# Kernel optimization log

Measured on AMD Instinct MI355X. Metric: run time of the kernel, lower is better.

## Reference

```python
import jax, jax.numpy as jnp
import numpy as np

B, C, H, W = 64, 256, 56, 56
SCALES = (1, 2, 4, 8)  # scale[:groups] with groups=4; sum = 15 pooled maps


def setup_inputs() -> dict:
    key = jax.random.key(0)
    k1, k2 = jax.random.split(key)
    x = jax.random.normal(k1, (B, C, H, W), dtype=jnp.float32)
    # weight: [num_fea=H*W, sum(scales)=15]; small init (original fills 0, which
    # would make the gate identically sigmoid(0)=0.5 — use small random instead)
    weight = jax.random.normal(k2, (H * W, 15), dtype=jnp.float32) * 0.02
    return {"x": x, "weight": weight}


def reference(x, weight):
    b, c, h, w = x.shape
    hw = h * w
    # Multi-scale channel-group mean pooling: for scale i, split channels into
    # i equal groups (c divisible by all scales) and mean over each group.
    # Equivalent to the original's loop of c*j//i : c*(j+1)//i slices.
    feats = [x.reshape(b, i, c // i, hw).mean(axis=2) for i in SCALES]
    t = jnp.concatenate(feats, axis=1)  # [b, 15, hw]
    # Points(): normalize across the 15 pooled features per spatial location
    mean = t.mean(axis=1, keepdims=True)           # [b, 1, hw]
    std = t.std(axis=1, keepdims=True)             # unbiased=False (ddof=0)
    tn = (t - mean) / std                          # [b, 15, hw]
    # _style_integration: per-pixel weighted sum over the 15 features
    z = jnp.einsum('bfs,sf->bs', tn, weight)       # [b, hw]
    gate = jax.nn.sigmoid(z).reshape(b, 1, h, w)
    return x * gate
```

## Files before the change

kernel.cpp:

```cpp
#include <hip/hip_runtime.h>
#include <math.h>


constexpr int C_   = 256;
constexpr int HW_  = 3136;
constexpr int T_   = 64;
constexpr int TPB_ = HW_ / T_;
constexpr int B_   = 64;

__global__ __launch_bounds__(256, 2) void ppca_fused(
    const float* __restrict__ x, const float* __restrict__ wgt,
    float* __restrict__ out)
{
  __shared__ __align__(16) float tile[C_ * T_];
  __shared__ float S[8 * T_];
  __shared__ float gate[T_];

  const int blk = blockIdx.x;
  const int b   = blk / TPB_;
  const int til = blk - b * TPB_;
  const int sp0 = til * T_;
  const size_t base = (size_t)b * C_ * HW_ + sp0;
  const float* xb = x + base;
  float* ob = out + base;

  const int t   = threadIdx.x;
  const int sp4 = t & 15;
  const int c0  = t >> 4;

  float4 v[16];
  #pragma unroll
  for (int i = 0; i < 16; ++i) {
    const int c = c0 + (i << 4);
    v[i] = *(const float4*)(xb + (size_t)c * HW_ + (sp4 << 2));
  }
  #pragma unroll
  for (int i = 0; i < 16; ++i) {
    const int c = c0 + (i << 4);
    *(float4*)(&tile[c * T_ + (sp4 << 2)]) = v[i];
  }
  __syncthreads();

  {
    const int w = t >> 6;
    const int l = t & 63;
    float s0 = 0.f, s1 = 0.f;
    #pragma unroll
    for (int k = 0; k < 32; ++k) s0 += tile[(w * 64 + k) * T_ + l];
    #pragma unroll
    for (int k = 0; k < 32; ++k) s1 += tile[(w * 64 + 32 + k) * T_ + l];
    S[(2 * w) * T_ + l]     = s0;
    S[(2 * w + 1) * T_ + l] = s1;
  }
  __syncthreads();

  if (t < T_) {
    float Sg[8];
    #pragma unroll
    for (int g = 0; g < 8; ++g) Sg[g] = S[g * T_ + t];
    float p64[4];
    #pragma unroll
    for (int j = 0; j < 4; ++j) p64[j] = Sg[2 * j] + Sg[2 * j + 1];
    const float p128a = p64[0] + p64[1];
    const float p128b = p64[2] + p64[3];
    const float tot   = p128a + p128b;

    float f[15];
    f[0] = tot * (1.f / 256.f);
    f[1] = p128a * (1.f / 128.f);
    f[2] = p128b * (1.f / 128.f);
    #pragma unroll
    for (int j = 0; j < 4; ++j) f[3 + j] = p64[j] * (1.f / 64.f);
    #pragma unroll
    for (int g = 0; g < 8; ++g) f[7 + g] = Sg[g] * (1.f / 32.f);

    float m = 0.f;
    #pragma unroll
    for (int i = 0; i < 15; ++i) m += f[i];
    m *= (1.f / 15.f);
    float var = 0.f;
    #pragma unroll
    for (int i = 0; i < 15; ++i) { const float d = f[i] - m; var += d * d; }
    var *= (1.f / 15.f);
    const float inv = 1.f / sqrtf(var);

    const float* wp = wgt + (size_t)(sp0 + t) * 15;
    float z = 0.f;
    #pragma unroll
    for (int i = 0; i < 15; ++i) z += (f[i] - m) * wp[i];
    z *= inv;
    gate[t] = 1.f / (1.f + __expf(-z));
  }
  __syncthreads();

  const float4 g4 = *(const float4*)(&gate[sp4 << 2]);
  #pragma unroll
  for (int i = 0; i < 16; ++i) {
    const int c = c0 + (i << 4);
    float4 vv = *(const float4*)(&tile[c * T_ + (sp4 << 2)]);
    vv.x *= g4.x; vv.y *= g4.y; vv.z *= g4.z; vv.w *= g4.w;
    *(float4*)(ob + (size_t)c * HW_ + (sp4 << 2)) = vv;
  }
}

extern "C" void kernel_launch(void* const* d_in, const int* in_sizes, int n_in,
                              void* d_out, int out_size, void* d_ws, size_t ws_size,
                              hipStream_t stream) {
  const float* x = (const float*)d_in[0];
  const float* w = (const float*)d_in[1];
  float* out = (float*)d_out;
  (void)in_sizes; (void)n_in; (void)out_size; (void)d_ws; (void)ws_size;

  dim3 grid(B_ * TPB_);
  dim3 block(256);
  ppca_fused<<<grid, block, 0, stream>>>(x, w, out);
}
```

Measured before the change: 337.5 us.

## Keep per-thread channel slices in registers and drop full LDS tile

Switches to 1024-thread blocks where each thread loads 4 channels for 4 spatial positions and keeps them in registers for the final gated store. Only 4-channel partial sums go to shared memory, replacing the 64 KB tile with a 16 KB buffer, and a reduction then forms the 8 group sums. This removes the LDS write/read round-trip of the whole tile and raises occupancy, at the cost of larger blocks with more barrier participants.

```diff
diff --git a/kernel.cpp b/kernel.cpp
--- a/kernel.cpp
+++ b/kernel.cpp
@@ -8,11 +8,11 @@
 constexpr int TPB_ = HW_ / T_;
 constexpr int B_   = 64;
 
-__global__ __launch_bounds__(256, 2) void ppca_fused(
+__global__ __launch_bounds__(1024, 8) void ppca_fused(
     const float* __restrict__ x, const float* __restrict__ wgt,
     float* __restrict__ out)
 {
-  __shared__ __align__(16) float tile[C_ * T_];
+  __shared__ __align__(16) float P[64 * T_];
   __shared__ float S[8 * T_];
   __shared__ float gate[T_];
 
@@ -26,31 +26,28 @@
 
   const int t   = threadIdx.x;
   const int sp4 = t & 15;
-  const int c0  = t >> 4;
+  const int cq  = t >> 4;
 
-  float4 v[16];
+  float4 v[4];
   #pragma unroll
-  for (int i = 0; i < 16; ++i) {
-    const int c = c0 + (i << 4);
-    v[i] = *(const float4*)(xb + (size_t)c * HW_ + (sp4 << 2));
-  }
-  #pragma unroll
-  for (int i = 0; i < 16; ++i) {
-    const int c = c0 + (i << 4);
-    *(float4*)(&tile[c * T_ + (sp4 << 2)]) = v[i];
-  }
+  for (int j = 0; j < 4; ++j)
+    v[j] = *(const float4*)(xb + (size_t)(4 * cq + j) * HW_ + (sp4 << 2));
+
+  float4 p;
+  p.x = (v[0].x + v[1].x) + (v[2].x + v[3].x);
+  p.y = (v[0].y + v[1].y) + (v[2].y + v[3].y);
+  p.z = (v[0].z + v[1].z) + (v[2].z + v[3].z);
+  p.w = (v[0].w + v[1].w) + (v[2].w + v[3].w);
+  *(float4*)(&P[cq * T_ + (sp4 << 2)]) = p;
   __syncthreads();
 
-  {
-    const int w = t >> 6;
-    const int l = t & 63;
-    float s0 = 0.f, s1 = 0.f;
+  if (t < 512) {
+    const int g = t >> 6;
+    const int s = t & 63;
+    float sum = 0.f;
     #pragma unroll
-    for (int k = 0; k < 32; ++k) s0 += tile[(w * 64 + k) * T_ + l];
-    #pragma unroll
-    for (int k = 0; k < 32; ++k) s1 += tile[(w * 64 + 32 + k) * T_ + l];
-    S[(2 * w) * T_ + l]     = s0;
-    S[(2 * w + 1) * T_ + l] = s1;
+    for (int k = 0; k < 8; ++k) sum += P[(8 * g + k) * T_ + s];
+    S[g * T_ + s] = sum;
   }
   __syncthreads();
 
@@ -95,11 +92,10 @@
 
   const float4 g4 = *(const float4*)(&gate[sp4 << 2]);
   #pragma unroll
-  for (int i = 0; i < 16; ++i) {
-    const int c = c0 + (i << 4);
-    float4 vv = *(const float4*)(&tile[c * T_ + (sp4 << 2)]);
+  for (int j = 0; j < 4; ++j) {
+    float4 vv = v[j];
     vv.x *= g4.x; vv.y *= g4.y; vv.z *= g4.z; vv.w *= g4.w;
-    *(float4*)(ob + (size_t)c * HW_ + (sp4 << 2)) = vv;
+    *(float4*)(ob + (size_t)(4 * cq + j) * HW_ + (sp4 << 2)) = vv;
   }
 }
 
@@ -112,6 +108,6 @@
   (void)in_sizes; (void)n_in; (void)out_size; (void)d_ws; (void)ws_size;
 
   dim3 grid(B_ * TPB_);
-  dim3 block(256);
+  dim3 block(1024);
   ppca_fused<<<grid, block, 0, stream>>>(x, w, out);
 }
```

Measured after the change: 339.5 us. Within noise of the previous version (+0.6%).
